# Kernel tuning notes

Hardware: AMD Instinct MI355X
Metric: run time of the kernel (lower is better)

Reference implementation:

```python
import jax, jax.numpy as jnp
import numpy as np

N = 100000
E = 600000
IN_DIM = 128
OUT_DIM = 256
BN_EPS = 1e-5


def setup_inputs() -> dict:
    key = jax.random.key(0)
    ks = jax.random.split(key, 12)
    x = jax.random.normal(ks[0], (N, IN_DIM), dtype=jnp.float32)
    edge_index = jax.random.randint(ks[1], (2, E), 0, N, dtype=jnp.int64)
    s1 = 1.0 / np.sqrt(IN_DIM)
    s2 = 1.0 / np.sqrt(OUT_DIM)
    return {
        "x": x,
        "edge_index": edge_index,
        "eps": jnp.zeros((), dtype=jnp.float32),  # GINConv eps init = 0
        "W1": jax.random.uniform(ks[2], (IN_DIM, OUT_DIM), jnp.float32, -s1, s1),
        "b1": jnp.zeros((OUT_DIM,), jnp.float32),
        "W2": jax.random.uniform(ks[3], (OUT_DIM, OUT_DIM), jnp.float32, -s2, s2),
        "b2": jnp.zeros((OUT_DIM,), jnp.float32),
        "gamma": jnp.ones((OUT_DIM,), jnp.float32),
        "beta": jnp.zeros((OUT_DIM,), jnp.float32),
        "run_mean": jnp.zeros((OUT_DIM,), jnp.float32),
        "run_var": jnp.ones((OUT_DIM,), jnp.float32),
        "Wp": jax.random.uniform(ks[4], (IN_DIM, OUT_DIM), jnp.float32, -s1, s1),
        "bp": jnp.zeros((OUT_DIM,), jnp.float32),
    }


def reference(x, edge_index, eps, W1, b1, W2, b2, gamma, beta, run_mean, run_var, Wp, bp):
    src, dst = edge_index[0], edge_index[1]
    # GIN aggregation: sum_{j in N(i)} x_j  (scatter-add of source features to dst)
    agg = jax.ops.segment_sum(x[src], dst, num_segments=N)
    h = (1.0 + eps) * x + agg            # [N, in_dim]
    # 2-layer MLP (nn1)
    h = jax.nn.relu(h @ W1 + b1) @ W2 + b2   # [N, out_dim]
    # BatchNorm1d (eval mode: running stats); dropout = identity (eval)
    h = (h - run_mean) * jax.lax.rsqrt(run_var + BN_EPS) * gamma + beta
    # residual with projection (in_dim != out_dim)
    return h + x @ Wp + bp
```

## Files before the change

### kernel.cpp

```cpp
#include <hip/hip_runtime.h>

#define N_ 100000
#define E_ 600000
#define IND_ 128
#define OUTD_ 256
#define NT_ (N_/16)
#define NB_ 98

typedef __attribute__((ext_vector_type(8))) short bf16x8;
typedef __attribute__((ext_vector_type(4))) float f32x4;
typedef __attribute__((ext_vector_type(2))) unsigned int u32x2;

static __device__ __forceinline__ unsigned f2bf_u(float f){
  union { float f; unsigned u; } v; v.f = f;
  return (v.u + 0x7fffu + ((v.u >> 16) & 1u)) >> 16;
}
static __device__ __forceinline__ unsigned pack2(float a, float b){
  return f2bf_u(a) | (f2bf_u(b) << 16);
}

__global__ void k_prep(const float* __restrict__ W1, const float* __restrict__ W2,
                       const float* __restrict__ Wp, const float* __restrict__ b2,
                       const float* __restrict__ gamma, const float* __restrict__ beta,
                       const float* __restrict__ mean, const float* __restrict__ var,
                       const float* __restrict__ bp,
                       unsigned short* __restrict__ W1s, unsigned short* __restrict__ W2s,
                       unsigned short* __restrict__ Wps,
                       float* __restrict__ scale, float* __restrict__ shift)
{
  int gid = blockIdx.x*256 + threadIdx.x;
  if (gid < 16384) {
    const float* W; unsigned short* Ws; int u;
    if (gid < 4096)       { W = W1; Ws = W1s; u = gid; }
    else if (gid < 12288) { W = W2; Ws = W2s; u = gid - 4096; }
    else                  { W = Wp; Ws = Wps; u = gid - 12288; }
    int l  = u & 63;
    int km = (u >> 6) & 1;
    int t  = (u >> 7) & 15;
    int q  = u >> 11;
    int kk = 2*q + km;
    int kb = kk*32 + (l >> 4)*8;
    int c  = 16*t + (l & 15);
    #pragma unroll
    for (int j = 0; j < 8; j++)
      Ws[u*8 + j] = (unsigned short)f2bf_u(W[(size_t)(kb + j)*OUTD_ + c]);
  } else if (gid < 16640) {
    int c = gid - 16384;
    float s = gamma[c] * rsqrtf(var[c] + 1e-5f);
    scale[c] = s;
    shift[c] = (b2[c] - mean[c]) * s + beta[c] + bp[c];
  }
}

__global__ void k_deg(const int* __restrict__ dst, int* __restrict__ deg){
  int e = blockIdx.x*256 + threadIdx.x;
  if (e < E_) atomicAdd(&deg[dst[e]], 1);
}

__global__ __launch_bounds__(1024) void k_scan1(const int* __restrict__ deg,
                                                int* __restrict__ bsum, int* __restrict__ offs){
  __shared__ int red[16];
  int tid = threadIdx.x;
  int i = blockIdx.x*1024 + tid;
  int v = (i < N_) ? deg[i] : 0;
  #pragma unroll
  for (int d = 32; d; d >>= 1) v += __shfl_down(v, d);
  if ((tid & 63) == 0) red[tid >> 6] = v;
  __syncthreads();
  if (tid < 16) {
    int s = red[tid];
    #pragma unroll
    for (int d = 8; d; d >>= 1) s += __shfl_down(s, d, 16);
    if (tid == 0) bsum[blockIdx.x] = s;
  }
  if (blockIdx.x == 0 && tid == 0) offs[N_] = E_;
}

__global__ __launch_bounds__(1024) void k_scan2(const int* __restrict__ deg,
                                                const int* __restrict__ bsum, int* __restrict__ offs){
  __shared__ int bs[128];
  __shared__ int d1[1024];
  int tid = threadIdx.x;
  if (tid < 128) bs[tid] = (tid < NB_) ? bsum[tid] : 0;
  __syncthreads();
  #pragma unroll
  for (int d = 1; d < 128; d <<= 1){
    int v = (tid < 128 && tid >= d) ? bs[tid - d] : 0;
    __syncthreads();
    if (tid < 128) bs[tid] += v;
    __syncthreads();
  }
  int bprefix = (blockIdx.x > 0) ? bs[blockIdx.x - 1] : 0;
  int i = blockIdx.x*1024 + tid;
  int v = (i < N_) ? deg[i] : 0;
  d1[tid] = v;
  __syncthreads();
  #pragma unroll
  for (int d = 1; d < 1024; d <<= 1){
    int t = (tid >= d) ? d1[tid - d] : 0;
    __syncthreads();
    d1[tid] += t;
    __syncthreads();
  }
  if (i < N_) offs[i] = bprefix + d1[tid] - v;
}

__global__ void k_fill(const int* __restrict__ src, const int* __restrict__ dst,
                       const int* __restrict__ offs, int* __restrict__ cur, int* __restrict__ adj){
  int e = blockIdx.x*256 + threadIdx.x;
  if (e < E_) {
    int d = dst[e];
    int p = atomicAdd(&cur[d], 1);
    adj[offs[d] + p] = src[e];
  }
}

__global__ void k_agg(const float* __restrict__ x, const int* __restrict__ offs,
                      const int* __restrict__ adj, const float* __restrict__ epsp,
                      unsigned* __restrict__ h0, unsigned* __restrict__ xb)
{
  int row  = blockIdx.x*4 + (threadIdx.x >> 6);
  int lane = threadIdx.x & 63;
  if (row >= N_) return;
  const float2* xr = (const float2*)(x + (size_t)row*IND_);
  float2 xv = xr[lane];
  float ax0=0.f, ay0=0.f, ax1=0.f, ay1=0.f, ax2=0.f, ay2=0.f, ax3=0.f, ay3=0.f;
  int b = offs[row], e = offs[row+1];
  for (int base = b; base < e; base += 64){
    int cnt = min(64, e - base);
    int idx = adj[base + min(lane, cnt - 1)];
    int j = 0;
    for (; j + 4 <= cnt; j += 4){
      int n0 = __shfl(idx, j+0);
      int n1 = __shfl(idx, j+1);
      int n2 = __shfl(idx, j+2);
      int n3 = __shfl(idx, j+3);
      float2 v0 = ((const float2*)(x + (size_t)n0*IND_))[lane];
      float2 v1 = ((const float2*)(x + (size_t)n1*IND_))[lane];
      float2 v2 = ((const float2*)(x + (size_t)n2*IND_))[lane];
      float2 v3 = ((const float2*)(x + (size_t)n3*IND_))[lane];
      ax0 += v0.x; ay0 += v0.y;
      ax1 += v1.x; ay1 += v1.y;
      ax2 += v2.x; ay2 += v2.y;
      ax3 += v3.x; ay3 += v3.y;
    }
    for (; j < cnt; j++){
      int n = __shfl(idx, j);
      float2 v = ((const float2*)(x + (size_t)n*IND_))[lane];
      ax0 += v.x; ay0 += v.y;
    }
  }
  float ax = (ax0 + ax1) + (ax2 + ax3);
  float ay = (ay0 + ay1) + (ay2 + ay3);
  float k1 = 1.f + epsp[0];
  h0[(size_t)row*64 + lane] = pack2(fmaf(k1, xv.x, ax), fmaf(k1, xv.y, ay));
  xb[(size_t)row*64 + lane] = pack2(xv.x, xv.y);
}

__global__ __launch_bounds__(256) void k_mlp1(const unsigned short* __restrict__ h0,
        const bf16x8* __restrict__ W1s, const float* __restrict__ b1,
        unsigned short* __restrict__ h1s)
{
  __shared__ bf16x8 w[2048];
  __shared__ __align__(16) char trans[4][2][1280];
  int tid = threadIdx.x;
  int wv = tid >> 6, lane = tid & 63, g = lane >> 4, r = lane & 15;
  int tile0 = blockIdx.x*4 + wv;
  int tile  = min(tile0, NT_ - 1);

  const bf16x8* hrow = (const bf16x8*)(h0 + ((size_t)tile*16 + r)*IND_);
  bf16x8 B[4];
  #pragma unroll
  for (int kk = 0; kk < 4; kk++) B[kk] = hrow[kk*4 + g];

  f32x4 acc[16];
  #pragma unroll
  for (int t = 0; t < 16; t++) acc[t] = (f32x4){0.f,0.f,0.f,0.f};

  for (int q = 0; q < 2; q++){
    __syncthreads();
    #pragma unroll
    for (int i = 0; i < 8; i++) w[tid + i*256] = W1s[q*2048 + tid + i*256];
    __syncthreads();
    #pragma unroll
    for (int km = 0; km < 2; km++){
      bf16x8 Bf = B[2*q + km];
      #pragma unroll
      for (int t = 0; t < 16; t++)
        acc[t] = __builtin_amdgcn_mfma_f32_16x16x32_bf16(w[(t*2+km)*64 + lane], Bf, acc[t], 0,0,0);
    }
  }

  const float4* b1v = (const float4*)b1;
  unsigned short* outp = h1s + (size_t)tile*4096;
  bool act = (tile0 < NT_);
  #pragma unroll
  for (int kkh = 0; kkh < 8; kkh++){
    char* tr = &trans[wv][kkh & 1][0];
    #pragma unroll
    for (int h = 0; h < 2; h++){
      int t = 2*kkh + h;
      float4 bb = b1v[t*4 + g];
      f32x4 a = acc[t];
      float v0 = fmaxf(a.x + bb.x, 0.f);
      float v1 = fmaxf(a.y + bb.y, 0.f);
      float v2 = fmaxf(a.z + bb.z, 0.f);
      float v3 = fmaxf(a.w + bb.w, 0.f);
      u32x2 dd; dd.x = pack2(v0, v1); dd.y = pack2(v2, v3);
      *(u32x2*)(tr + r*80 + h*32 + g*8) = dd;
    }
    bf16x8 frag = *(const bf16x8*)(tr + r*80 + g*16);
    if (act) *(bf16x8*)(outp + (kkh*64 + lane)*8) = frag;
  }
}

__global__ __launch_bounds__(256) void k_mlp2(const bf16x8* __restrict__ h1s,
        const unsigned short* __restrict__ xb,
        const bf16x8* __restrict__ W2s, const bf16x8* __restrict__ Wps,
        const float* __restrict__ scale, const float* __restrict__ shift,
        float* __restrict__ out)
{
  __shared__ bf16x8 w[2048];
  int tid = threadIdx.x, wv = tid >> 6, lane = tid & 63, g = lane >> 4, r = lane & 15;
  int tile0 = blockIdx.x*4 + wv;
  int tile  = min(tile0, NT_ - 1);
  const bf16x8* h1f  = h1s + (size_t)tile*512;
  const bf16x8* xrow = (const bf16x8*)(xb + ((size_t)tile*16 + r)*IND_);

  f32x4 acc[16];
  #pragma unroll
  for (int t = 0; t < 16; t++) acc[t] = (f32x4){0.f,0.f,0.f,0.f};

  for (int q = 0; q < 4; q++){
    __syncthreads();
    #pragma unroll
    for (int i = 0; i < 8; i++) w[tid + i*256] = W2s[q*2048 + tid + i*256];
    __syncthreads();
    #pragma unroll
    for (int km = 0; km < 2; km++){
      bf16x8 Bf = h1f[(2*q + km)*64 + lane];
      #pragma unroll
      for (int t = 0; t < 16; t++)
        acc[t] = __builtin_amdgcn_mfma_f32_16x16x32_bf16(w[(t*2+km)*64 + lane], Bf, acc[t], 0,0,0);
    }
  }
  for (int q = 0; q < 2; q++){
    __syncthreads();
    #pragma unroll
    for (int i = 0; i < 8; i++) w[tid + i*256] = Wps[q*2048 + tid + i*256];
    __syncthreads();
    #pragma unroll
    for (int km = 0; km < 2; km++){
      bf16x8 Bf = xrow[(2*q + km)*4 + g];
      #pragma unroll
      for (int t = 0; t < 16; t++)
        acc[t] = __builtin_amdgcn_mfma_f32_16x16x32_bf16(w[(t*2+km)*64 + lane], Bf, acc[t], 0,0,0);
    }
  }

  if (tile0 < NT_){
    const float4* sc = (const float4*)scale;
    const float4* sh = (const float4*)shift;
    #pragma unroll
    for (int t = 0; t < 16; t++){
      float4 s = sc[t*4 + g], b = sh[t*4 + g];
      f32x4 a = acc[t];
      float4 o;
      o.x = fmaf(a.x, s.x, b.x);
      o.y = fmaf(a.y, s.y, b.y);
      o.z = fmaf(a.z, s.z, b.z);
      o.w = fmaf(a.w, s.w, b.w);
      *(float4*)(out + ((size_t)tile*16 + r)*OUTD_ + t*16 + g*4) = o;
    }
  }
}

extern "C" void kernel_launch(void* const* d_in, const int* in_sizes, int n_in,
                              void* d_out, int out_size, void* d_ws, size_t ws_size,
                              hipStream_t stream)
{
  const float* x     = (const float*)d_in[0];
  const int*   ei    = (const int*)d_in[1];
  const float* eps   = (const float*)d_in[2];
  const float* W1    = (const float*)d_in[3];
  const float* b1    = (const float*)d_in[4];
  const float* W2    = (const float*)d_in[5];
  const float* b2    = (const float*)d_in[6];
  const float* gamma = (const float*)d_in[7];
  const float* beta  = (const float*)d_in[8];
  const float* rmean = (const float*)d_in[9];
  const float* rvar  = (const float*)d_in[10];
  const float* Wp    = (const float*)d_in[11];
  const float* bp    = (const float*)d_in[12];
  float* out = (float*)d_out;

  char* ws = (char*)d_ws; size_t off = 0;
  auto carve = [&](size_t b)->char* { char* p = ws + off; off = (off + b + 255) & ~(size_t)255; return p; };
  unsigned*       h0    = (unsigned*)carve((size_t)N_*IND_*2);
  unsigned*       xbuf  = (unsigned*)carve((size_t)N_*IND_*2);
  unsigned short* h1s   = (unsigned short*)carve((size_t)N_*OUTD_*2);
  unsigned short* W1s   = (unsigned short*)carve(4096*16);
  unsigned short* W2s   = (unsigned short*)carve(8192*16);
  unsigned short* Wps   = (unsigned short*)carve(4096*16);
  float*          scale = (float*)carve(256*4);
  float*          shift = (float*)carve(256*4);
  int*            deg   = (int*)carve((size_t)N_*4);
  int*            cur   = (int*)carve((size_t)N_*4);
  int*            offs  = (int*)carve((size_t)(N_+1)*4);
  int*            adj   = (int*)carve((size_t)E_*4);
  int*            bsum  = (int*)carve((size_t)NB_*4);

  hipMemsetAsync(deg, 0, (size_t)N_*4, stream);
  hipMemsetAsync(cur, 0, (size_t)N_*4, stream);

  k_prep <<<65, 256, 0, stream>>>(W1, W2, Wp, b2, gamma, beta, rmean, rvar, bp,
                                  W1s, W2s, Wps, scale, shift);
  k_deg  <<<(E_+255)/256, 256, 0, stream>>>(ei + E_, deg);
  k_scan1<<<NB_, 1024, 0, stream>>>(deg, bsum, offs);
  k_scan2<<<NB_, 1024, 0, stream>>>(deg, bsum, offs);
  k_fill <<<(E_+255)/256, 256, 0, stream>>>(ei, ei + E_, offs, cur, adj);
  k_agg  <<<(N_+3)/4, 256, 0, stream>>>(x, offs, adj, eps, h0, xbuf);
  k_mlp1 <<<(NT_+3)/4, 256, 0, stream>>>((const unsigned short*)h0, (const bf16x8*)W1s, b1, h1s);
  k_mlp2 <<<(NT_+3)/4, 256, 0, stream>>>((const bf16x8*)h1s, (const unsigned short*)xbuf,
                                         (const bf16x8*)W2s, (const bf16x8*)Wps, scale, shift, out);
}
```

Baseline: 214.1 us.

## Fuse aggregation and both MLP GEMMs into one kernel over bf16 x

Casts x to bf16 once in the prep kernel. A single fused kernel then gathers neighbour rows from the bf16 copy, builds the 16-row h0 tile in shared memory, and runs both MLP layers plus the residual projection with the intermediate kept in registers. This removes the h0 and h1 round trips through global memory and two kernel launches, and halves gather traffic. The cost is that each wave now handles 16 rows of aggregation one after another, which reduces gather parallelism. Neighbour sums are also taken from bf16-rounded x, which loses some precision.

```diff
diff --git a/kernel.cpp b/kernel.cpp
--- a/kernel.cpp
+++ b/kernel.cpp
@@ -6,6 +6,7 @@
 #define OUTD_ 256
 #define NT_ (N_/16)
 #define NB_ 98
+#define CASTN_ (N_*IND_/2)
 
 typedef __attribute__((ext_vector_type(8))) short bf16x8;
 typedef __attribute__((ext_vector_type(4))) float f32x4;
@@ -18,15 +19,23 @@
 static __device__ __forceinline__ unsigned pack2(float a, float b){
   return f2bf_u(a) | (f2bf_u(b) << 16);
 }
-
-__global__ void k_prep(const float* __restrict__ W1, const float* __restrict__ W2,
+static __device__ __forceinline__ float blo(unsigned u){
+  union { unsigned u; float f; } v; v.u = u << 16; return v.f;
+}
+static __device__ __forceinline__ float bhi(unsigned u){
+  union { unsigned u; float f; } v; v.u = u & 0xffff0000u; return v.f;
+}
+
+__global__ void k_prep(const float* __restrict__ x,
+                       const float* __restrict__ W1, const float* __restrict__ W2,
                        const float* __restrict__ Wp, const float* __restrict__ b2,
                        const float* __restrict__ gamma, const float* __restrict__ beta,
                        const float* __restrict__ mean, const float* __restrict__ var,
                        const float* __restrict__ bp,
                        unsigned short* __restrict__ W1s, unsigned short* __restrict__ W2s,
                        unsigned short* __restrict__ Wps,
-                       float* __restrict__ scale, float* __restrict__ shift)
+                       float* __restrict__ scale, float* __restrict__ shift,
+                       unsigned* __restrict__ xbw)
 {
   int gid = blockIdx.x*256 + threadIdx.x;
   if (gid < 16384) {
@@ -49,6 +58,10 @@
     float s = gamma[c] * rsqrtf(var[c] + 1e-5f);
     scale[c] = s;
     shift[c] = (b2[c] - mean[c]) * s + beta[c] + bp[c];
+  } else if (gid < 16640 + CASTN_) {
+    int ci = gid - 16640;
+    float2 v = ((const float2*)x)[ci];
+    xbw[ci] = pack2(v.x, v.y);
   }
 }
 
@@ -115,63 +128,62 @@
   }
 }
 
-__global__ void k_agg(const float* __restrict__ x, const int* __restrict__ offs,
-                      const int* __restrict__ adj, const float* __restrict__ epsp,
-                      unsigned* __restrict__ h0, unsigned* __restrict__ xb)
-{
-  int row  = blockIdx.x*4 + (threadIdx.x >> 6);
-  int lane = threadIdx.x & 63;
-  if (row >= N_) return;
-  const float2* xr = (const float2*)(x + (size_t)row*IND_);
-  float2 xv = xr[lane];
-  float ax0=0.f, ay0=0.f, ax1=0.f, ay1=0.f, ax2=0.f, ay2=0.f, ax3=0.f, ay3=0.f;
-  int b = offs[row], e = offs[row+1];
-  for (int base = b; base < e; base += 64){
-    int cnt = min(64, e - base);
-    int idx = adj[base + min(lane, cnt - 1)];
-    int j = 0;
-    for (; j + 4 <= cnt; j += 4){
-      int n0 = __shfl(idx, j+0);
-      int n1 = __shfl(idx, j+1);
-      int n2 = __shfl(idx, j+2);
-      int n3 = __shfl(idx, j+3);
-      float2 v0 = ((const float2*)(x + (size_t)n0*IND_))[lane];
-      float2 v1 = ((const float2*)(x + (size_t)n1*IND_))[lane];
-      float2 v2 = ((const float2*)(x + (size_t)n2*IND_))[lane];
-      float2 v3 = ((const float2*)(x + (size_t)n3*IND_))[lane];
-      ax0 += v0.x; ay0 += v0.y;
-      ax1 += v1.x; ay1 += v1.y;
-      ax2 += v2.x; ay2 += v2.y;
-      ax3 += v3.x; ay3 += v3.y;
-    }
-    for (; j < cnt; j++){
-      int n = __shfl(idx, j);
-      float2 v = ((const float2*)(x + (size_t)n*IND_))[lane];
-      ax0 += v.x; ay0 += v.y;
-    }
-  }
-  float ax = (ax0 + ax1) + (ax2 + ax3);
-  float ay = (ay0 + ay1) + (ay2 + ay3);
-  float k1 = 1.f + epsp[0];
-  h0[(size_t)row*64 + lane] = pack2(fmaf(k1, xv.x, ax), fmaf(k1, xv.y, ay));
-  xb[(size_t)row*64 + lane] = pack2(xv.x, xv.y);
-}
-
-__global__ __launch_bounds__(256) void k_mlp1(const unsigned short* __restrict__ h0,
+__global__ __launch_bounds__(256, 2) void k_fused(
+        const unsigned* __restrict__ xb32,
+        const unsigned short* __restrict__ xb16,
+        const int* __restrict__ offs, const int* __restrict__ adj,
+        const float* __restrict__ epsp,
         const bf16x8* __restrict__ W1s, const float* __restrict__ b1,
-        unsigned short* __restrict__ h1s)
+        const bf16x8* __restrict__ W2s, const bf16x8* __restrict__ Wps,
+        const float* __restrict__ scale, const float* __restrict__ shift,
+        float* __restrict__ out)
 {
   __shared__ bf16x8 w[2048];
-  __shared__ __align__(16) char trans[4][2][1280];
-  int tid = threadIdx.x;
-  int wv = tid >> 6, lane = tid & 63, g = lane >> 4, r = lane & 15;
+  __shared__ __align__(16) unsigned exch[4][1088];
+  int tid = threadIdx.x, wv = tid >> 6, lane = tid & 63, g = lane >> 4, r = lane & 15;
   int tile0 = blockIdx.x*4 + wv;
   int tile  = min(tile0, NT_ - 1);
-
-  const bf16x8* hrow = (const bf16x8*)(h0 + ((size_t)tile*16 + r)*IND_);
+  float k1 = 1.f + epsp[0];
+
+  for (int rr = 0; rr < 16; rr++){
+    int row = tile*16 + rr;
+    unsigned xw = xb32[(size_t)row*64 + lane];
+    float ax0=0.f, ay0=0.f, ax1=0.f, ay1=0.f, ax2=0.f, ay2=0.f, ax3=0.f, ay3=0.f;
+    int b = offs[row], e = offs[row+1];
+    for (int base = b; base < e; base += 64){
+      int cnt = min(64, e - base);
+      int idx = adj[base + min(lane, cnt - 1)];
+      int j = 0;
+      for (; j + 4 <= cnt; j += 4){
+        int n0 = __shfl(idx, j+0), n1 = __shfl(idx, j+1);
+        int n2 = __shfl(idx, j+2), n3 = __shfl(idx, j+3);
+        unsigned v0 = xb32[(size_t)n0*64 + lane];
+        unsigned v1 = xb32[(size_t)n1*64 + lane];
+        unsigned v2 = xb32[(size_t)n2*64 + lane];
+        unsigned v3 = xb32[(size_t)n3*64 + lane];
+        ax0 += blo(v0); ay0 += bhi(v0);
+        ax1 += blo(v1); ay1 += bhi(v1);
+        ax2 += blo(v2); ay2 += bhi(v2);
+        ax3 += blo(v3); ay3 += bhi(v3);
+      }
+      for (; j < cnt; j++){
+        int n = __shfl(idx, j);
+        unsigned v = xb32[(size_t)n*64 + lane];
+        ax0 += blo(v); ay0 += bhi(v);
+      }
+    }
+    float ax = (ax0 + ax1) + (ax2 + ax3);
+    float ay = (ay0 + ay1) + (ay2 + ay3);
+    exch[wv][rr*68 + lane] = pack2(fmaf(k1, blo(xw), ax), fmaf(k1, bhi(xw), ay));
+  }
   bf16x8 B[4];
   #pragma unroll
-  for (int kk = 0; kk < 4; kk++) B[kk] = hrow[kk*4 + g];
+  for (int kk = 0; kk < 4; kk++)
+    B[kk] = *(const bf16x8*)&exch[wv][r*68 + kk*16 + g*4];
+  const bf16x8* xrowf = (const bf16x8*)(xb16 + ((size_t)tile*16 + r)*IND_);
+  bf16x8 XV[4];
+  #pragma unroll
+  for (int kk = 0; kk < 4; kk++) XV[kk] = xrowf[kk*4 + g];
 
   f32x4 acc[16];
   #pragma unroll
@@ -192,11 +204,10 @@
   }
 
   const float4* b1v = (const float4*)b1;
-  unsigned short* outp = h1s + (size_t)tile*4096;
-  bool act = (tile0 < NT_);
+  bf16x8 H[8];
   #pragma unroll
   for (int kkh = 0; kkh < 8; kkh++){
-    char* tr = &trans[wv][kkh & 1][0];
+    char* tr = (char*)&exch[wv][0] + (kkh & 1)*1280;
     #pragma unroll
     for (int h = 0; h < 2; h++){
       int t = 2*kkh + h;
@@ -209,25 +220,9 @@
       u32x2 dd; dd.x = pack2(v0, v1); dd.y = pack2(v2, v3);
       *(u32x2*)(tr + r*80 + h*32 + g*8) = dd;
     }
-    bf16x8 frag = *(const bf16x8*)(tr + r*80 + g*16);
-    if (act) *(bf16x8*)(outp + (kkh*64 + lane)*8) = frag;
-  }
-}
-
-__global__ __launch_bounds__(256) void k_mlp2(const bf16x8* __restrict__ h1s,
-        const unsigned short* __restrict__ xb,
-        const bf16x8* __restrict__ W2s, const bf16x8* __restrict__ Wps,
-        const float* __restrict__ scale, const float* __restrict__ shift,
-        float* __restrict__ out)
-{
-  __shared__ bf16x8 w[2048];
-  int tid = threadIdx.x, wv = tid >> 6, lane = tid & 63, g = lane >> 4, r = lane & 15;
-  int tile0 = blockIdx.x*4 + wv;
-  int tile  = min(tile0, NT_ - 1);
-  const bf16x8* h1f  = h1s + (size_t)tile*512;
-  const bf16x8* xrow = (const bf16x8*)(xb + ((size_t)tile*16 + r)*IND_);
-
-  f32x4 acc[16];
+    H[kkh] = *(const bf16x8*)(tr + r*80 + g*16);
+  }
+
   #pragma unroll
   for (int t = 0; t < 16; t++) acc[t] = (f32x4){0.f,0.f,0.f,0.f};
 
@@ -238,7 +233,7 @@
     __syncthreads();
     #pragma unroll
     for (int km = 0; km < 2; km++){
-      bf16x8 Bf = h1f[(2*q + km)*64 + lane];
+      bf16x8 Bf = H[2*q + km];
       #pragma unroll
       for (int t = 0; t < 16; t++)
         acc[t] = __builtin_amdgcn_mfma_f32_16x16x32_bf16(w[(t*2+km)*64 + lane], Bf, acc[t], 0,0,0);
@@ -251,7 +246,7 @@
     __syncthreads();
     #pragma unroll
     for (int km = 0; km < 2; km++){
-      bf16x8 Bf = xrow[(2*q + km)*4 + g];
+      bf16x8 Bf = XV[2*q + km];
       #pragma unroll
       for (int t = 0; t < 16; t++)
         acc[t] = __builtin_amdgcn_mfma_f32_16x16x32_bf16(w[(t*2+km)*64 + lane], Bf, acc[t], 0,0,0);
@@ -296,9 +291,7 @@
 
   char* ws = (char*)d_ws; size_t off = 0;
   auto carve = [&](size_t b)->char* { char* p = ws + off; off = (off + b + 255) & ~(size_t)255; return p; };
-  unsigned*       h0    = (unsigned*)carve((size_t)N_*IND_*2);
-  unsigned*       xbuf  = (unsigned*)carve((size_t)N_*IND_*2);
-  unsigned short* h1s   = (unsigned short*)carve((size_t)N_*OUTD_*2);
+  unsigned*       xbuf  = (unsigned*)carve((size_t)CASTN_*4);
   unsigned short* W1s   = (unsigned short*)carve(4096*16);
   unsigned short* W2s   = (unsigned short*)carve(8192*16);
   unsigned short* Wps   = (unsigned short*)carve(4096*16);
@@ -313,14 +306,13 @@
   hipMemsetAsync(deg, 0, (size_t)N_*4, stream);
   hipMemsetAsync(cur, 0, (size_t)N_*4, stream);
 
-  k_prep <<<65, 256, 0, stream>>>(W1, W2, Wp, b2, gamma, beta, rmean, rvar, bp,
-                                  W1s, W2s, Wps, scale, shift);
+  k_prep <<<(16640 + CASTN_ + 255)/256, 256, 0, stream>>>(x, W1, W2, Wp, b2, gamma, beta,
+                                  rmean, rvar, bp, W1s, W2s, Wps, scale, shift, xbuf);
   k_deg  <<<(E_+255)/256, 256, 0, stream>>>(ei + E_, deg);
   k_scan1<<<NB_, 1024, 0, stream>>>(deg, bsum, offs);
   k_scan2<<<NB_, 1024, 0, stream>>>(deg, bsum, offs);
   k_fill <<<(E_+255)/256, 256, 0, stream>>>(ei, ei + E_, offs, cur, adj);
-  k_agg  <<<(N_+3)/4, 256, 0, stream>>>(x, offs, adj, eps, h0, xbuf);
-  k_mlp1 <<<(NT_+3)/4, 256, 0, stream>>>((const unsigned short*)h0, (const bf16x8*)W1s, b1, h1s);
-  k_mlp2 <<<(NT_+3)/4, 256, 0, stream>>>((const bf16x8*)h1s, (const unsigned short*)xbuf,
-                                         (const bf16x8*)W2s, (const bf16x8*)Wps, scale, shift, out);
-}
+  k_fused<<<(NT_+3)/4, 256, 0, stream>>>(xbuf, (const unsigned short*)xbuf, offs, adj, eps,
+                                         (const bf16x8*)W1s, b1, (const bf16x8*)W2s,
+                                         (const bf16x8*)Wps, scale, shift, out);
+}
```

New measurement: 265.0 us. +23.8%, slower.
